# Optimization experiments

Measured on AMD Instinct MI355X. Metric: run time of the kernel, lower is better.

## Reference

```python
import jax, jax.numpy as jnp
import numpy as np

B, S, C, H, HS = 4, 2048, 1024, 16, 64


def setup_inputs() -> dict:
    key = jax.random.key(0)
    ks = jax.random.split(key, 5)
    scale = 0.02
    x = jax.random.normal(ks[0], (B, S, C), dtype=jnp.float32)
    Wq = jax.random.normal(ks[1], (H, C, HS), dtype=jnp.float32) * scale
    Wk = jax.random.normal(ks[2], (H, C, HS), dtype=jnp.float32) * scale
    Wv = jax.random.normal(ks[3], (H, C, HS), dtype=jnp.float32) * scale
    Wp = jax.random.normal(ks[4], (C, C), dtype=jnp.float32) * scale
    bp = jnp.zeros((C,), dtype=jnp.float32)
    return {"x": x, "Wq": Wq, "Wk": Wk, "Wv": Wv, "Wp": Wp, "bp": bp}


def reference(x, Wq, Wk, Wv, Wp, bp):
    # Batched equivalent of the per-head Python loop: project all heads at once.
    q = jnp.einsum('bsc,hcd->bhsd', x, Wq)  # [B,H,S,HS]
    k = jnp.einsum('bsc,hcd->bhsd', x, Wk)
    v = jnp.einsum('bsc,hcd->bhsd', x, Wv)
    att = jnp.einsum('bsd,btd->bst'.replace('b', 'bh'), q, k) if False else jnp.einsum('bhsd,bhtd->bhst', q, k)
    att = att * (1.0 / jnp.sqrt(jnp.float32(HS)))  # k.shape[-1]**-0.5 scaling
    causal = jnp.tril(jnp.ones((S, S), dtype=bool))
    att = jnp.where(causal, att, jnp.finfo(att.dtype).min)
    att = jax.nn.softmax(att, axis=-1)
    # attention dropout / proj dropout are identity in eval mode
    out = jnp.einsum('bhst,bhtd->bhsd', att, v)          # [B,H,S,HS]
    out = out.transpose(0, 2, 1, 3).reshape(B, S, C)      # concat heads
    return out @ Wp.T + bp                                # final projection
```

## Files before the change

kernel.cpp:

```cpp
#include <hip/hip_runtime.h>
#include <hip/hip_bf16.h>
#include <math.h>


typedef __bf16 bf16_t;
typedef __bf16 bf16x4_t __attribute__((ext_vector_type(4)));
typedef __bf16 bf16x8 __attribute__((ext_vector_type(8)));
typedef __bf16 bf16x2 __attribute__((ext_vector_type(2)));
typedef float f32x4 __attribute__((ext_vector_type(4)));
typedef float f32x16 __attribute__((ext_vector_type(16)));

#define S_LEN 2048
#define C_DIM 1024
#define NHEAD 16
#define HS_DIM 64
#define MROWS 8192
#define QSCALE 0.18033688011112042f

__device__ __forceinline__ void cvt8(bf16_t* dst, const float* __restrict__ src) {
  const float4 a = *(const float4*)src;
  const float4 b = *(const float4*)(src + 4);
  bf16x8 v;
  v[0] = (bf16_t)a.x; v[1] = (bf16_t)a.y; v[2] = (bf16_t)a.z; v[3] = (bf16_t)a.w;
  v[4] = (bf16_t)b.x; v[5] = (bf16_t)b.y; v[6] = (bf16_t)b.z; v[7] = (bf16_t)b.w;
  *(bf16x8*)dst = v;
}

__device__ __forceinline__ unsigned int pk2(float a, float b) {
  union { bf16x2 h; unsigned int u; } t;
  t.h[0] = (bf16_t)a;
  t.h[1] = (bf16_t)b;
  return t.u;
}

__device__ __forceinline__ void gload16(const bf16_t* g, bf16_t* l) {
  __builtin_amdgcn_global_load_lds(
      (const __attribute__((address_space(1))) unsigned int*)(const void*)g,
      (__attribute__((address_space(3))) unsigned int*)(void*)l,
      16, 0, 0);
}

#define SBAR()  { __builtin_amdgcn_sched_barrier(0); \
                  __builtin_amdgcn_s_barrier();      \
                  __builtin_amdgcn_sched_barrier(0); }
#define VMCNT(N) { asm volatile("s_waitcnt vmcnt(" #N ")" ::: "memory"); \
                   __builtin_amdgcn_sched_barrier(0); }
#define LGKMCNT0() { asm volatile("s_waitcnt lgkmcnt(0)" ::: "memory"); \
                     __builtin_amdgcn_sched_barrier(0); }

__global__ __launch_bounds__(256) void convert_bf16(
    const float* __restrict__ src, bf16_t* __restrict__ dst) {
  const size_t i = ((size_t)blockIdx.x * 256 + threadIdx.x) * 8;
  cvt8(dst + i, src + i);
}

__global__ __launch_bounds__(256) void pack_w_kernel(
    const float* __restrict__ Wq, const float* __restrict__ Wk,
    const float* __restrict__ Wv, bf16_t* __restrict__ WT) {
  __shared__ __align__(16) float tile[64][68];
  const int wsel = blockIdx.z;
  const int h = blockIdx.y;
  const int c0 = blockIdx.x * 64;
  const float* W = (wsel == 0 ? Wq : (wsel == 1 ? Wk : Wv)) + (size_t)h * (C_DIM * HS_DIM);
  const int tr = threadIdx.x >> 2;
  const int tc = (threadIdx.x & 3) << 4;
  #pragma unroll
  for (int j = 0; j < 16; j += 4)
    *(float4*)&tile[tr][tc + j] = *(const float4*)(W + (size_t)(c0 + tr) * HS_DIM + tc + j);
  __syncthreads();
  const int d = threadIdx.x >> 2;
  const int cb = (threadIdx.x & 3) << 4;
  bf16_t* dst = WT + ((size_t)(wsel * 1024 + h * 64 + d)) * C_DIM + c0 + cb;
  #pragma unroll
  for (int i = 0; i < 16; ++i) dst[i] = (bf16_t)tile[cb + i][d];
}

__global__ __launch_bounds__(256, 2) void gemm_qkv128(
    const bf16_t* __restrict__ A, const bf16_t* __restrict__ WT,
    bf16_t* __restrict__ Q, bf16_t* __restrict__ K, bf16_t* __restrict__ VT) {
  __shared__ __align__(16) bf16_t As[2][128 * 64];
  __shared__ __align__(16) bf16_t Bs[2][128 * 64];
  const int m0 = blockIdx.x * 128;
  const int n0 = blockIdx.y * 128;
  const int tid = threadIdx.x;
  const int wave = tid >> 6, lane = tid & 63, quad = lane >> 4, lid = lane & 15;
  const int ww = wave >> 1, wc = wave & 1;
  const int lr = lane >> 3;
  const int lc = (lane & 7) << 3;

  const bf16_t* Ag = A  + (size_t)m0 * C_DIM;
  const bf16_t* Bg = WT + (size_t)n0 * C_DIM;

  f32x4 acc[4][4] = {};

  #define STAGE_QKV(D, KT)                                                   \
    {                                                                        \
      const int k0_ = (KT) * 64;                                             \
      _Pragma("unroll")                                                      \
      for (int j = 0; j < 4; ++j) {                                          \
        const int row_ = wave * 32 + j * 8;                                  \
        gload16(Ag + (size_t)(row_ + lr) * C_DIM + k0_ + lc, &As[D][row_ * 64]); \
        gload16(Bg + (size_t)(row_ + lr) * C_DIM + k0_ + lc, &Bs[D][row_ * 64]); \
      }                                                                      \
    }

  STAGE_QKV(0, 0)
  STAGE_QKV(1, 1)

  #pragma unroll 1
  for (int kt = 0; kt < 16; ++kt) {
    const int d = kt & 1;
    if (kt < 15) { VMCNT(8) } else { VMCNT(0) }
    SBAR()

    const bf16_t* Asd = As[d];
    const bf16_t* Bsd = Bs[d];
    bf16x8 af[2][4], bfr[2][4];
    #pragma unroll
    for (int c = 0; c < 2; ++c) {
      #pragma unroll
      for (int mt = 0; mt < 4; ++mt)
        af[c][mt] = *(const bf16x8*)&Asd[(ww * 64 + mt * 16 + lid) * 64 + c * 32 + quad * 8];
      #pragma unroll
      for (int nt = 0; nt < 4; ++nt)
        bfr[c][nt] = *(const bf16x8*)&Bsd[(wc * 64 + nt * 16 + lid) * 64 + c * 32 + quad * 8];
    }
    LGKMCNT0()
    SBAR()

    if (kt + 2 < 16) {
      if (d == 0) { STAGE_QKV(0, kt + 2) } else { STAGE_QKV(1, kt + 2) }
    }
    __builtin_amdgcn_sched_barrier(0);

    #pragma unroll
    for (int c = 0; c < 2; ++c)
      #pragma unroll
      for (int mt = 0; mt < 4; ++mt)
        #pragma unroll
        for (int nt = 0; nt < 4; ++nt)
          acc[mt][nt] = __builtin_amdgcn_mfma_f32_16x16x32_bf16(af[c][mt], bfr[c][nt], acc[mt][nt], 0, 0, 0);
  }

  const int wsel = n0 >> 10;
  const float qs = (wsel == 0) ? QSCALE : 1.0f;
  #pragma unroll
  for (int mt = 0; mt < 4; ++mt) {
    #pragma unroll
    for (int nt = 0; nt < 4; ++nt) {
      const int row0 = m0 + ww * 64 + mt * 16 + quad * 4;
      const int col = n0 + wc * 64 + nt * 16 + lid;
      const int h = (col >> 6) & 15, dd = col & 63;
      if (wsel == 2) {
        bf16x4_t pv;
        #pragma unroll
        for (int r = 0; r < 4; ++r) pv[r] = (bf16_t)acc[mt][nt][r];
        const int b = row0 >> 11, s = row0 & 2047;
        *(bf16x4_t*)&VT[((size_t)(b * NHEAD + h) * HS_DIM + dd) * S_LEN + s] = pv;
      } else {
        bf16_t* dst = (wsel == 0 ? Q : K);
        #pragma unroll
        for (int r = 0; r < 4; ++r)
          dst[(size_t)(row0 + r) * C_DIM + h * HS_DIM + dd] = (bf16_t)(acc[mt][nt][r] * qs);
      }
    }
  }
}

#define PACK_GROUP(SV, BASE, FR)                                         \
  {                                                                      \
    unsigned int w0 = pk2(SV[BASE + 0], SV[BASE + 1]);                   \
    unsigned int w1 = pk2(SV[BASE + 2], SV[BASE + 3]);                   \
    unsigned int w2 = pk2(SV[BASE + 4], SV[BASE + 5]);                   \
    unsigned int w3 = pk2(SV[BASE + 6], SV[BASE + 7]);                   \
    auto sA = __builtin_amdgcn_permlane32_swap(w0, w2, false, false);    \
    auto sB = __builtin_amdgcn_permlane32_swap(w1, w3, false, false);    \
    FR.u[0] = sA[0]; FR.u[2] = sA[1];                                    \
    FR.u[1] = sB[0]; FR.u[3] = sB[1];                                    \
  }

union PFrag { bf16x8 v; unsigned int u[4]; };

__global__ __launch_bounds__(512, 4) void flash_attn_kernel(
    const bf16_t* __restrict__ Q,
    const bf16_t* __restrict__ Kb,
    const bf16_t* __restrict__ VT,
    bf16_t* __restrict__ O) {
  __shared__ __align__(16) bf16_t Ks[2][64][64];
  __shared__ __align__(16) bf16_t Vs[2][64][64];
  const int id = blockIdx.x;
  const int bh = id & 63;
  const int g = id >> 6;
  const int p = ((g & 3) << 1) | (g >> 2);
  const int b = bh >> 4, h = bh & 15;
  const int rb = b * S_LEN;
  const int tid = threadIdx.x;
  const int wave = tid >> 6, lane = tid & 63;
  const int l31 = lane & 31, hi = lane >> 5;

  const int myTile = (wave < 4) ? (15 - p) : p;
  const int qw = myTile * 128 + (wave & 3) * 32;

  const int srow = tid >> 3;
  const int scol = (tid & 7) << 3;
  const int swcol = scol ^ ((srow & 7) << 3);
  const int rsw = (lane & 7) << 3;

  const bf16_t* kbase = Kb + (size_t)(rb + srow) * C_DIM + h * HS_DIM + scol;
  const bf16_t* vbase = VT + ((size_t)bh * HS_DIM + srow) * S_LEN + scol;

  bf16x8 qfrag[4];
  {
    const bf16_t* qp = Q + (size_t)(rb + qw + l31) * C_DIM + h * HS_DIM + hi * 8;
    #pragma unroll
    for (int c = 0; c < 4; ++c) qfrag[c] = *(const bf16x8*)(qp + c * 16);
  }

  f32x16 oacc0 = {}, oacc1 = {};
  float m_i = -INFINITY, l_i = 0.f;
  const int nIter = 2 * (15 - p) + 2;

  {
    uint4 k0 = *(const uint4*)(kbase);
    uint4 v0 = *(const uint4*)(vbase);
    *(uint4*)&Ks[0][srow][swcol] = k0;
    *(uint4*)&Vs[0][srow][swcol] = v0;
  }
  __syncthreads();

  for (int i = 0; i < nIter; ++i) {
    const int pb = i & 1;
    const int t0 = i << 6;

    uint4 k0r, v0r;
    const bool haveNext = (i + 1 < nIter);
    if (haveNext) {
      k0r = *(const uint4*)(kbase + (size_t)(t0 + 64) * C_DIM);
      v0r = *(const uint4*)(vbase + (t0 + 64));
    }

    if (t0 < qw + 32) {
      f32x16 sa0 = {}, sa1 = {};
      __builtin_amdgcn_s_setprio(1);
      #pragma unroll
      for (int c = 0; c < 4; ++c) {
        const int col = (c * 16 + hi * 8) ^ rsw;
        bf16x8 kf0 = *(const bf16x8*)&Ks[pb][l31][col];
        bf16x8 kf1 = *(const bf16x8*)&Ks[pb][l31 + 32][col];
        sa0 = __builtin_amdgcn_mfma_f32_32x32x16_bf16(kf0, qfrag[c], sa0, 0, 0, 0);
        sa1 = __builtin_amdgcn_mfma_f32_32x32x16_bf16(kf1, qfrag[c], sa1, 0, 0, 0);
      }
      __builtin_amdgcn_s_setprio(0);

      const bool diag = (t0 + 63 > qw);
      if (diag) {
        const int qg = qw + l31;
        #pragma unroll
        for (int r = 0; r < 16; ++r) {
          const int tr = (r & 3) + 8 * (r >> 2) + 4 * hi;
          if (t0 + tr > qg)      sa0[r] = -INFINITY;
          if (t0 + 32 + tr > qg) sa1[r] = -INFINITY;
        }
      }

      float pmax = -INFINITY;
      #pragma unroll
      for (int r = 0; r < 16; ++r) pmax = fmaxf(pmax, fmaxf(sa0[r], sa1[r]));
      pmax = fmaxf(pmax, __shfl_xor(pmax, 32));

      if (!__all(pmax <= m_i + 8.f)) {
        const float mnew = fmaxf(m_i, pmax);
        const float alpha = exp2f(m_i - mnew);
        m_i = mnew;
        l_i *= alpha;
        #pragma unroll
        for (int r = 0; r < 16; ++r) {
          const float av = __shfl(alpha, (r & 3) + 8 * (r >> 2) + 4 * hi);
          oacc0[r] *= av;
          oacc1[r] *= av;
        }
      }

      float rsum = 0.f;
      #pragma unroll
      for (int r = 0; r < 16; ++r) {
        const float p0 = exp2f(sa0[r] - m_i);
        const float p1 = exp2f(sa1[r] - m_i);
        sa0[r] = p0; sa1[r] = p1;
        rsum += p0 + p1;
      }
      rsum += __shfl_xor(rsum, 32);
      l_i += rsum;

      PFrag pf[4];
      PACK_GROUP(sa0, 0, pf[0])
      PACK_GROUP(sa0, 8, pf[1])
      PACK_GROUP(sa1, 0, pf[2])
      PACK_GROUP(sa1, 8, pf[3])

      __builtin_amdgcn_s_setprio(1);
      #pragma unroll
      for (int ks = 0; ks < 4; ++ks) {
        const int col = (ks * 16 + hi * 8) ^ rsw;
        bf16x8 vf0 = *(const bf16x8*)&Vs[pb][l31][col];
        bf16x8 vf1 = *(const bf16x8*)&Vs[pb][l31 + 32][col];
        oacc0 = __builtin_amdgcn_mfma_f32_32x32x16_bf16(pf[ks].v, vf0, oacc0, 0, 0, 0);
        oacc1 = __builtin_amdgcn_mfma_f32_32x32x16_bf16(pf[ks].v, vf1, oacc1, 0, 0, 0);
      }
      __builtin_amdgcn_s_setprio(0);
    }

    if (haveNext) {
      *(uint4*)&Ks[1 - pb][srow][swcol] = k0r;
      *(uint4*)&Vs[1 - pb][srow][swcol] = v0r;
      __syncthreads();
    }
  }

  const float linv = 1.f / l_i;
  #pragma unroll
  for (int r = 0; r < 16; ++r) {
    const int qrow = (r & 3) + 8 * (r >> 2) + 4 * hi;
    const float inv = __shfl(linv, qrow);
    const int row = rb + qw + qrow;
    O[(size_t)row * C_DIM + h * HS_DIM + l31]      = (bf16_t)(oacc0[r] * inv);
    O[(size_t)row * C_DIM + h * HS_DIM + 32 + l31] = (bf16_t)(oacc1[r] * inv);
  }
}

__global__ __launch_bounds__(256, 2) void gemm_out128(
    const bf16_t* __restrict__ A,
    const bf16_t* __restrict__ Bw,
    const float* __restrict__ bias,
    float* __restrict__ out) {
  __shared__ __align__(16) bf16_t As[2][128 * 64];
  __shared__ __align__(16) bf16_t Bs[2][128 * 64];
  const int m0 = blockIdx.x * 128;
  const int n0 = blockIdx.y * 128;
  const int tid = threadIdx.x;
  const int wave = tid >> 6, lane = tid & 63, quad = lane >> 4, lid = lane & 15;
  const int ww = wave >> 1, wc = wave & 1;
  const int lr = lane >> 3;
  const int lc = (lane & 7) << 3;

  const bf16_t* Ag = A  + (size_t)m0 * C_DIM;
  const bf16_t* Bg = Bw + (size_t)n0 * C_DIM;

  f32x4 acc[4][4] = {};

  #define STAGE_OUT(D, KT)                                                   \
    {                                                                        \
      const int k0_ = (KT) * 64;                                             \
      _Pragma("unroll")                                                      \
      for (int j = 0; j < 4; ++j) {                                          \
        const int row_ = wave * 32 + j * 8;                                  \
        gload16(Ag + (size_t)(row_ + lr) * C_DIM + k0_ + lc, &As[D][row_ * 64]); \
        gload16(Bg + (size_t)(row_ + lr) * C_DIM + k0_ + lc, &Bs[D][row_ * 64]); \
      }                                                                      \
    }

  STAGE_OUT(0, 0)
  STAGE_OUT(1, 1)

  #pragma unroll 1
  for (int kt = 0; kt < 16; ++kt) {
    const int d = kt & 1;
    if (kt < 15) { VMCNT(8) } else { VMCNT(0) }
    SBAR()

    const bf16_t* Asd = As[d];
    const bf16_t* Bsd = Bs[d];
    bf16x8 af[2][4], bfr[2][4];
    #pragma unroll
    for (int c = 0; c < 2; ++c) {
      #pragma unroll
      for (int mt = 0; mt < 4; ++mt)
        af[c][mt] = *(const bf16x8*)&Asd[(ww * 64 + mt * 16 + lid) * 64 + c * 32 + quad * 8];
      #pragma unroll
      for (int nt = 0; nt < 4; ++nt)
        bfr[c][nt] = *(const bf16x8*)&Bsd[(wc * 64 + nt * 16 + lid) * 64 + c * 32 + quad * 8];
    }
    LGKMCNT0()
    SBAR()

    if (kt + 2 < 16) {
      if (d == 0) { STAGE_OUT(0, kt + 2) } else { STAGE_OUT(1, kt + 2) }
    }
    __builtin_amdgcn_sched_barrier(0);

    #pragma unroll
    for (int c = 0; c < 2; ++c)
      #pragma unroll
      for (int mt = 0; mt < 4; ++mt)
        #pragma unroll
        for (int nt = 0; nt < 4; ++nt)
          acc[mt][nt] = __builtin_amdgcn_mfma_f32_16x16x32_bf16(af[c][mt], bfr[c][nt], acc[mt][nt], 0, 0, 0);
  }

  #pragma unroll
  for (int mt = 0; mt < 4; ++mt) {
    #pragma unroll
    for (int nt = 0; nt < 4; ++nt) {
      #pragma unroll
      for (int r = 0; r < 4; ++r) {
        const int row = m0 + ww * 64 + mt * 16 + quad * 4 + r;
        const int col = n0 + wc * 64 + nt * 16 + lid;
        out[(size_t)row * C_DIM + col] = acc[mt][nt][r] + bias[col];
      }
    }
  }
}

extern "C" void kernel_launch(void* const* d_in, const int* in_sizes, int n_in,
                              void* d_out, int out_size, void* d_ws, size_t ws_size,
                              hipStream_t stream) {
  const float *x, *Wq, *Wk, *Wv, *Wp, *bp;
  if (in_sizes[0] == MROWS * C_DIM) {
    x  = (const float*)d_in[0];
    Wq = (const float*)d_in[1];
    Wk = (const float*)d_in[2];
    Wv = (const float*)d_in[3];
    Wp = (const float*)d_in[4];
    bp = (const float*)d_in[5];
  } else {
    Wk = (const float*)d_in[0];
    Wp = (const float*)d_in[1];
    Wq = (const float*)d_in[2];
    Wv = (const float*)d_in[3];
    bp = (const float*)d_in[4];
    x  = (const float*)d_in[5];
  }
  float* out = (float*)d_out;

  const size_t NB = (size_t)MROWS * C_DIM;
  bf16_t* ws  = (bf16_t*)d_ws;
  bf16_t* Ob  = ws;
  bf16_t* WT  = ws;
  bf16_t* Qb  = ws + NB;
  bf16_t* Kb  = Qb + NB;
  bf16_t* VTb = Kb + NB;
  bf16_t* WpT = Qb;
  bf16_t* xb  = (bf16_t*)d_out;

  pack_w_kernel<<<dim3(16, 16, 3), 256, 0, stream>>>(Wq, Wk, Wv, WT);
  convert_bf16<<<dim3(4096), 256, 0, stream>>>(x, xb);
  gemm_qkv128<<<dim3(64, 24), 256, 0, stream>>>(xb, WT, Qb, Kb, VTb);
  flash_attn_kernel<<<dim3(512), 512, 0, stream>>>(Qb, Kb, VTb, Ob);
  convert_bf16<<<dim3(512), 256, 0, stream>>>(Wp, WpT);
  gemm_out128<<<dim3(64, 8), 256, 0, stream>>>(Ob, WpT, bp, out);
}
```

Measured before the change: 258.3 us.

## Load K/V tiles directly into LDS and split key tiles into 32-row halves

Replaces the register-staged K/V prefetch with direct global-to-LDS loads through a gload16 helper. Swizzling moves from the LDS store address to the global source address, which frees registers and removes the separate LDS store step. The attention loop now processes each 64-key tile as two 32-key halves, so fully masked halves on the causal diagonal are skipped and live score registers shrink. The cost is more softmax rescale and reduction steps per tile, plus reliance on the async loads completing before the barrier.

```diff
diff --git a/kernel.cpp b/kernel.cpp
--- a/kernel.cpp
+++ b/kernel.cpp
@@ -202,12 +202,13 @@
   const int qw = myTile * 128 + (wave & 3) * 32;
 
   const int srow = tid >> 3;
-  const int scol = (tid & 7) << 3;
-  const int swcol = scol ^ ((srow & 7) << 3);
+  const int lc = (tid & 7) << 3;
+  const int ssc = lc ^ ((srow & 7) << 3);
   const int rsw = (lane & 7) << 3;
 
-  const bf16_t* kbase = Kb + (size_t)(rb + srow) * C_DIM + h * HS_DIM + scol;
-  const bf16_t* vbase = VT + ((size_t)bh * HS_DIM + srow) * S_LEN + scol;
+  const bf16_t* kbase = Kb + (size_t)(rb + srow) * C_DIM + h * HS_DIM + ssc;
+  const bf16_t* vbase = VT + ((size_t)bh * HS_DIM + srow) * S_LEN + ssc;
+  const int w8 = wave * 8;
 
   bf16x8 qfrag[4];
   {
@@ -220,101 +221,91 @@
   float m_i = -INFINITY, l_i = 0.f;
   const int nIter = 2 * (15 - p) + 2;
 
-  {
-    uint4 k0 = *(const uint4*)(kbase);
-    uint4 v0 = *(const uint4*)(vbase);
-    *(uint4*)&Ks[0][srow][swcol] = k0;
-    *(uint4*)&Vs[0][srow][swcol] = v0;
-  }
+  gload16(kbase, &Ks[0][w8][0]);
+  gload16(vbase, &Vs[0][w8][0]);
   __syncthreads();
 
   for (int i = 0; i < nIter; ++i) {
     const int pb = i & 1;
     const int t0 = i << 6;
-
-    uint4 k0r, v0r;
     const bool haveNext = (i + 1 < nIter);
+
     if (haveNext) {
-      k0r = *(const uint4*)(kbase + (size_t)(t0 + 64) * C_DIM);
-      v0r = *(const uint4*)(vbase + (t0 + 64));
-    }
-
-    if (t0 < qw + 32) {
-      f32x16 sa0 = {}, sa1 = {};
-      __builtin_amdgcn_s_setprio(1);
-      #pragma unroll
-      for (int c = 0; c < 4; ++c) {
-        const int col = (c * 16 + hi * 8) ^ rsw;
-        bf16x8 kf0 = *(const bf16x8*)&Ks[pb][l31][col];
-        bf16x8 kf1 = *(const bf16x8*)&Ks[pb][l31 + 32][col];
-        sa0 = __builtin_amdgcn_mfma_f32_32x32x16_bf16(kf0, qfrag[c], sa0, 0, 0, 0);
-        sa1 = __builtin_amdgcn_mfma_f32_32x32x16_bf16(kf1, qfrag[c], sa1, 0, 0, 0);
+      gload16(kbase + (size_t)(t0 + 64) * C_DIM, &Ks[1 - pb][w8][0]);
+      gload16(vbase + (t0 + 64),                 &Vs[1 - pb][w8][0]);
+    }
+
+    #pragma unroll
+    for (int hh = 0; hh < 2; ++hh) {
+      const int tb = t0 + 32 * hh;
+      if (tb < qw + 32) {
+        f32x16 sa = {};
+        __builtin_amdgcn_s_setprio(1);
+        #pragma unroll
+        for (int c = 0; c < 4; ++c) {
+          const int col = (c * 16 + hi * 8) ^ rsw;
+          bf16x8 kf = *(const bf16x8*)&Ks[pb][l31 + 32 * hh][col];
+          sa = __builtin_amdgcn_mfma_f32_32x32x16_bf16(kf, qfrag[c], sa, 0, 0, 0);
+        }
+        __builtin_amdgcn_s_setprio(0);
+
+        const bool diag = (tb + 31 > qw);
+        if (diag) {
+          const int qg = qw + l31;
+          #pragma unroll
+          for (int r = 0; r < 16; ++r) {
+            const int tr = (r & 3) + 8 * (r >> 2) + 4 * hi;
+            if (tb + tr > qg) sa[r] = -INFINITY;
+          }
+        }
+
+        float pmax = -INFINITY;
+        #pragma unroll
+        for (int r = 0; r < 16; ++r) pmax = fmaxf(pmax, sa[r]);
+        pmax = fmaxf(pmax, __shfl_xor(pmax, 32));
+
+        if (!__all(pmax <= m_i + 8.f)) {
+          const float mnew = fmaxf(m_i, pmax);
+          const float alpha = exp2f(m_i - mnew);
+          m_i = mnew;
+          l_i *= alpha;
+          #pragma unroll
+          for (int r = 0; r < 16; ++r) {
+            const float av = __shfl(alpha, (r & 3) + 8 * (r >> 2) + 4 * hi);
+            oacc0[r] *= av;
+            oacc1[r] *= av;
+          }
+        }
+
+        float rsum = 0.f;
+        #pragma unroll
+        for (int r = 0; r < 16; ++r) {
+          const float pv = exp2f(sa[r] - m_i);
+          sa[r] = pv;
+          rsum += pv;
+        }
+        rsum += __shfl_xor(rsum, 32);
+        l_i += rsum;
+
+        PFrag pf0, pf1;
+        PACK_GROUP(sa, 0, pf0)
+        PACK_GROUP(sa, 8, pf1)
+
+        __builtin_amdgcn_s_setprio(1);
+        #pragma unroll
+        for (int ks2 = 0; ks2 < 2; ++ks2) {
+          const int col = ((2 * hh + ks2) * 16 + hi * 8) ^ rsw;
+          bf16x8 vf0 = *(const bf16x8*)&Vs[pb][l31][col];
+          bf16x8 vf1 = *(const bf16x8*)&Vs[pb][l31 + 32][col];
+          const bf16x8 pv = (ks2 == 0) ? pf0.v : pf1.v;
+          oacc0 = __builtin_amdgcn_mfma_f32_32x32x16_bf16(pv, vf0, oacc0, 0, 0, 0);
+          oacc1 = __builtin_amdgcn_mfma_f32_32x32x16_bf16(pv, vf1, oacc1, 0, 0, 0);
+        }
+        __builtin_amdgcn_s_setprio(0);
       }
-      __builtin_amdgcn_s_setprio(0);
-
-      const bool diag = (t0 + 63 > qw);
-      if (diag) {
-        const int qg = qw + l31;
-        #pragma unroll
-        for (int r = 0; r < 16; ++r) {
-          const int tr = (r & 3) + 8 * (r >> 2) + 4 * hi;
-          if (t0 + tr > qg)      sa0[r] = -INFINITY;
-          if (t0 + 32 + tr > qg) sa1[r] = -INFINITY;
-        }
-      }
-
-      float pmax = -INFINITY;
-      #pragma unroll
-      for (int r = 0; r < 16; ++r) pmax = fmaxf(pmax, fmaxf(sa0[r], sa1[r]));
-      pmax = fmaxf(pmax, __shfl_xor(pmax, 32));
-
-      if (!__all(pmax <= m_i + 8.f)) {
-        const float mnew = fmaxf(m_i, pmax);
-        const float alpha = exp2f(m_i - mnew);
-        m_i = mnew;
-        l_i *= alpha;
-        #pragma unroll
-        for (int r = 0; r < 16; ++r) {
-          const float av = __shfl(alpha, (r & 3) + 8 * (r >> 2) + 4 * hi);
-          oacc0[r] *= av;
-          oacc1[r] *= av;
-        }
-      }
-
-      float rsum = 0.f;
-      #pragma unroll
-      for (int r = 0; r < 16; ++r) {
-        const float p0 = exp2f(sa0[r] - m_i);
-        const float p1 = exp2f(sa1[r] - m_i);
-        sa0[r] = p0; sa1[r] = p1;
-        rsum += p0 + p1;
-      }
-      rsum += __shfl_xor(rsum, 32);
-      l_i += rsum;
-
-      PFrag pf[4];
-      PACK_GROUP(sa0, 0, pf[0])
-      PACK_GROUP(sa0, 8, pf[1])
-      PACK_GROUP(sa1, 0, pf[2])
-      PACK_GROUP(sa1, 8, pf[3])
-
-      __builtin_amdgcn_s_setprio(1);
-      #pragma unroll
-      for (int ks = 0; ks < 4; ++ks) {
-        const int col = (ks * 16 + hi * 8) ^ rsw;
-        bf16x8 vf0 = *(const bf16x8*)&Vs[pb][l31][col];
-        bf16x8 vf1 = *(const bf16x8*)&Vs[pb][l31 + 32][col];
-        oacc0 = __builtin_amdgcn_mfma_f32_32x32x16_bf16(pf[ks].v, vf0, oacc0, 0, 0, 0);
-        oacc1 = __builtin_amdgcn_mfma_f32_32x32x16_bf16(pf[ks].v, vf1, oacc1, 0, 0, 0);
-      }
-      __builtin_amdgcn_s_setprio(0);
-    }
-
-    if (haveNext) {
-      *(uint4*)&Ks[1 - pb][srow][swcol] = k0r;
-      *(uint4*)&Vs[1 - pb][srow][swcol] = v0r;
-      __syncthreads();
-    }
+    }
+
+    if (haveNext) __syncthreads();
   }
 
   const float linv = 1.f / l_i;
```

Result: slower. 263.8 us (+2.2%).

## Use direct global-to-LDS loads for K/V and tree-reduce softmax max/sum

Applied to the files above, without the earlier changes.

Replaces the register-staged K/V tile loads with global_load_lds, swizzling on the global side so the LDS layout stays XOR-swizzled, which removes VGPR staging and the LDS write instructions. Rewrites the per-row max and sum reductions as balanced trees and uses permlane32_swap instead of a shuffle for the cross-half reduction. Also changes the mapping of block index to causal tile pair. There is a risk the loop has no explicit vmcnt wait before the barrier, so correctness depends on __syncthreads or compiler waits covering the async LDS loads.

```diff
diff --git a/kernel.cpp b/kernel.cpp
--- a/kernel.cpp
+++ b/kernel.cpp
@@ -31,6 +31,19 @@
   t.h[0] = (bf16_t)a;
   t.h[1] = (bf16_t)b;
   return t.u;
+}
+
+__device__ __forceinline__ float xmax32(float v) {
+  union { float f; unsigned int u; } a; a.f = v;
+  auto s = __builtin_amdgcn_permlane32_swap(a.u, a.u, false, false);
+  union { unsigned int u; float f; } lo, hi; lo.u = s[0]; hi.u = s[1];
+  return fmaxf(lo.f, hi.f);
+}
+__device__ __forceinline__ float xadd32(float v) {
+  union { float f; unsigned int u; } a; a.f = v;
+  auto s = __builtin_amdgcn_permlane32_swap(a.u, a.u, false, false);
+  union { unsigned int u; float f; } lo, hi; lo.u = s[0]; hi.u = s[1];
+  return lo.f + hi.f;
 }
 
 __device__ __forceinline__ void gload16(const bf16_t* g, bf16_t* l) {
@@ -191,7 +204,7 @@
   const int id = blockIdx.x;
   const int bh = id & 63;
   const int g = id >> 6;
-  const int p = ((g & 3) << 1) | (g >> 2);
+  const int p = (g < 4) ? g : (11 - g);
   const int b = bh >> 4, h = bh & 15;
   const int rb = b * S_LEN;
   const int tid = threadIdx.x;
@@ -202,12 +215,13 @@
   const int qw = myTile * 128 + (wave & 3) * 32;
 
   const int srow = tid >> 3;
-  const int scol = (tid & 7) << 3;
-  const int swcol = scol ^ ((srow & 7) << 3);
+  const int lcol = (tid & 7) << 3;
+  const int ssc = lcol ^ ((srow & 7) << 3);
   const int rsw = (lane & 7) << 3;
 
-  const bf16_t* kbase = Kb + (size_t)(rb + srow) * C_DIM + h * HS_DIM + scol;
-  const bf16_t* vbase = VT + ((size_t)bh * HS_DIM + srow) * S_LEN + scol;
+  const bf16_t* kbase = Kb + (size_t)(rb + srow) * C_DIM + h * HS_DIM + ssc;
+  const bf16_t* vbase = VT + ((size_t)bh * HS_DIM + srow) * S_LEN + ssc;
+  const int w8 = wave * 8;
 
   bf16x8 qfrag[4];
   {
@@ -220,23 +234,18 @@
   float m_i = -INFINITY, l_i = 0.f;
   const int nIter = 2 * (15 - p) + 2;
 
-  {
-    uint4 k0 = *(const uint4*)(kbase);
-    uint4 v0 = *(const uint4*)(vbase);
-    *(uint4*)&Ks[0][srow][swcol] = k0;
-    *(uint4*)&Vs[0][srow][swcol] = v0;
-  }
+  gload16(kbase, &Ks[0][w8][0]);
+  gload16(vbase, &Vs[0][w8][0]);
   __syncthreads();
 
   for (int i = 0; i < nIter; ++i) {
     const int pb = i & 1;
     const int t0 = i << 6;
-
-    uint4 k0r, v0r;
     const bool haveNext = (i + 1 < nIter);
+
     if (haveNext) {
-      k0r = *(const uint4*)(kbase + (size_t)(t0 + 64) * C_DIM);
-      v0r = *(const uint4*)(vbase + (t0 + 64));
+      gload16(kbase + (size_t)(t0 + 64) * C_DIM, &Ks[1 - pb][w8][0]);
+      gload16(vbase + (t0 + 64),                 &Vs[1 - pb][w8][0]);
     }
 
     if (t0 < qw + 32) {
@@ -263,10 +272,14 @@
         }
       }
 
-      float pmax = -INFINITY;
-      #pragma unroll
-      for (int r = 0; r < 16; ++r) pmax = fmaxf(pmax, fmaxf(sa0[r], sa1[r]));
-      pmax = fmaxf(pmax, __shfl_xor(pmax, 32));
+      float tm[8];
+      #pragma unroll
+      for (int r = 0; r < 8; ++r)
+        tm[r] = fmaxf(fmaxf(sa0[r], sa0[r + 8]), fmaxf(sa1[r], sa1[r + 8]));
+      #pragma unroll
+      for (int r = 0; r < 4; ++r) tm[r] = fmaxf(tm[r], tm[r + 4]);
+      float pmax = fmaxf(fmaxf(tm[0], tm[1]), fmaxf(tm[2], tm[3]));
+      pmax = xmax32(pmax);
 
       if (!__all(pmax <= m_i + 8.f)) {
         const float mnew = fmaxf(m_i, pmax);
@@ -281,15 +294,19 @@
         }
       }
 
-      float rsum = 0.f;
       #pragma unroll
       for (int r = 0; r < 16; ++r) {
-        const float p0 = exp2f(sa0[r] - m_i);
-        const float p1 = exp2f(sa1[r] - m_i);
-        sa0[r] = p0; sa1[r] = p1;
-        rsum += p0 + p1;
-      }
-      rsum += __shfl_xor(rsum, 32);
+        sa0[r] = exp2f(sa0[r] - m_i);
+        sa1[r] = exp2f(sa1[r] - m_i);
+      }
+      float ts[8];
+      #pragma unroll
+      for (int r = 0; r < 8; ++r)
+        ts[r] = (sa0[r] + sa0[r + 8]) + (sa1[r] + sa1[r + 8]);
+      #pragma unroll
+      for (int r = 0; r < 4; ++r) ts[r] += ts[r + 4];
+      float rsum = (ts[0] + ts[1]) + (ts[2] + ts[3]);
+      rsum = xadd32(rsum);
       l_i += rsum;
 
       PFrag pf[4];
@@ -310,11 +327,7 @@
       __builtin_amdgcn_s_setprio(0);
     }
 
-    if (haveNext) {
-      *(uint4*)&Ks[1 - pb][srow][swcol] = k0r;
-      *(uint4*)&Vs[1 - pb][srow][swcol] = v0r;
-      __syncthreads();
-    }
+    if (haveNext) __syncthreads();
   }
 
   const float linv = 1.f / l_i;
```

Result: no change. 257.4 us (-0.3%).
